# Optimization experiments

Hardware: AMD Instinct MI355X
Metric: run time of the kernel (lower is better)

Reference implementation:

```python
import jax, jax.numpy as jnp
import numpy as np

K = 1024      # num_embeddings
D = 256       # embedding_dim
B, T = 64, 2048
DECAY = 0.99
EPS = 1e-5
COMMIT = 0.25


def setup_inputs() -> dict:
    key = jax.random.key(0)
    k1, k2, k3 = jax.random.split(key, 3)
    inputs = jax.random.normal(k1, (D, B, T), dtype=jnp.float32)
    embedding = jax.random.normal(k2, (K, D), dtype=jnp.float32)        # nn.Embedding weight (normal_())
    ema_w = jax.random.normal(k3, (K, D), dtype=jnp.float32)            # _ema_w (normal_())
    ema_cluster_size = jnp.zeros((K,), dtype=jnp.float32)               # _ema_cluster_size buffer
    return {"inputs": inputs, "embedding": embedding,
            "ema_cluster_size": ema_cluster_size, "ema_w": ema_w}


def reference(inputs, embedding, ema_cluster_size, ema_w):
    # inputs: [D, B, T] -> permute(1,2,0) -> [B, T, D]
    x = jnp.transpose(inputs, (1, 2, 0))
    flat = x.reshape(-1, D)                                  # [N, D], N = B*T

    # squared-euclidean distances to codebook: [N, K]
    distances = (jnp.sum(flat * flat, axis=1, keepdims=True)
                 + jnp.sum(embedding * embedding, axis=1)
                 - 2.0 * (flat @ embedding.T))

    encoding_indices = jnp.argmin(distances, axis=1)         # [N]
    encodings = jax.nn.one_hot(encoding_indices, K, dtype=jnp.float32)  # [N, K]

    # --- EMA codebook update (training path; detached in torch via nn.Parameter rewrap) ---
    counts = jnp.sum(encodings, axis=0)                      # [K]
    new_cs = ema_cluster_size * DECAY + (1.0 - DECAY) * counts
    n = jnp.sum(new_cs)
    new_cs = (new_cs + EPS) / (n + K * EPS) * n              # Laplace smoothing
    dw = encodings.T @ flat                                  # [K, D] scatter-add of assigned vectors
    new_ema_w = ema_w * DECAY + (1.0 - DECAY) * dw
    new_embedding = new_ema_w / new_cs[:, None]              # updated codebook

    # quantize with the UPDATED codebook (as in the torch training path)
    quantized = (encodings @ new_embedding).reshape(x.shape)  # [B, T, D]

    e_latent_loss = jnp.mean((jax.lax.stop_gradient(quantized) - x) ** 2)
    vq_loss = COMMIT * e_latent_loss

    # straight-through estimator
    quantized_st = x + jax.lax.stop_gradient(quantized - x)

    avg_probs = jnp.mean(encodings, axis=0)                  # [K]
    perplexity = jnp.exp(-jnp.sum(avg_probs * jnp.log(avg_probs + 1e-10)))

    quantized_out = jnp.transpose(quantized_st, (2, 0, 1))   # back to [D, B, T]
    return (vq_loss, quantized_out, perplexity, encodings, distances,
            encoding_indices, new_cs, new_ema_w, new_embedding)
```

## Files before the change

kernel.cpp:

```cpp
#include <hip/hip_runtime.h>
#include <hip/hip_bf16.h>
#include <cstdint>
#include <cstddef>

#define N_ROWS 131072
#define K_CB   1024
#define D_DIM  256
#define ND_TOT 33554432ull
#define NK_TOT 134217728ull
#define CHUNK  64

typedef __attribute__((ext_vector_type(8))) short short8;
typedef __attribute__((ext_vector_type(4))) float f32x4;
typedef __attribute__((address_space(3))) uint32_t lds_u32_t;
typedef const __attribute__((address_space(1))) uint32_t glb_u32_t;

static __device__ __forceinline__ float omd() { return (float)(1.0 - 0.99); }

static __device__ __forceinline__ float bf2f(ushort u) {
  union { uint32_t i; float f; } x; x.i = ((uint32_t)u) << 16; return x.f;
}
static __device__ __forceinline__ ushort f2bf(float f) {
  uint32_t x = __builtin_bit_cast(uint32_t, f);
  return (ushort)((x + 0x7fffu + ((x >> 16) & 1u)) >> 16);
}
static __device__ __forceinline__ void split3(float v, ushort& h, ushort& m, ushort& l) {
  h = f2bf(v);
  float r1 = v - bf2f(h);
  m = f2bf(r1);
  l = f2bf(r1 - bf2f(m));
}

__global__ __launch_bounds__(256) void split_a_k(const float* __restrict__ in,
    ushort* __restrict__ aH, ushort* __restrict__ aM, ushort* __restrict__ aL,
    float* __restrict__ xsq) {
  __shared__ float tile[128][65];
  __shared__ float part[4][64];
  int n0 = blockIdx.x * 64, d0 = blockIdx.y * 128;
  int lane = threadIdx.x & 63, grp = threadIdx.x >> 6;
  float ps = 0.f;
#pragma unroll
  for (int r = 0; r < 32; ++r) {
    int d = grp * 32 + r;
    float v = in[(size_t)(d0 + d) * N_ROWS + n0 + lane];
    tile[d][lane] = v;
    ps += v * v;
  }
  part[grp][lane] = ps;
  __syncthreads();
  if (grp == 0) {
    float s = part[0][lane] + part[1][lane] + part[2][lane] + part[3][lane];
    atomicAdd(&xsq[n0 + lane], s);
  }
#pragma unroll
  for (int r = 0; r < 16; ++r) {
    int nr = grp * 16 + r;
    float v0 = tile[lane * 2][nr], v1 = tile[lane * 2 + 1][nr];
    ushort h0, m0, l0, h1, m1, l1;
    split3(v0, h0, m0, l0);
    split3(v1, h1, m1, l1);
    size_t o = (size_t)(n0 + nr) * D_DIM + d0 + lane * 2;
    *(uint32_t*)&aH[o] = (uint32_t)h0 | ((uint32_t)h1 << 16);
    *(uint32_t*)&aM[o] = (uint32_t)m0 | ((uint32_t)m1 << 16);
    *(uint32_t*)&aL[o] = (uint32_t)l0 | ((uint32_t)l1 << 16);
  }
}

__global__ __launch_bounds__(256) void split_b_esq_k(const float* __restrict__ emb,
    ushort* __restrict__ bH, ushort* __restrict__ bM, float* __restrict__ esq) {
  int k = blockIdx.x * 4 + (threadIdx.x >> 6);
  int lane = threadIdx.x & 63;
  const float* er = emb + (size_t)k * D_DIM;
  float s = 0.f;
#pragma unroll
  for (int j = 0; j < 4; ++j) {
    float v = er[j * 64 + lane];
    ushort h, m, l;
    split3(v, h, m, l);
    bH[(size_t)k * D_DIM + j * 64 + lane] = h;
    bM[(size_t)k * D_DIM + j * 64 + lane] = m;
    s += v * v;
  }
  for (int off = 32; off; off >>= 1) s += __shfl_down(s, off);
  if (lane == 0) esq[k] = s;
}

__global__ __launch_bounds__(512, 1) void mfma_dist_k(
    const ushort* __restrict__ aH, const ushort* __restrict__ aM,
    const ushort* __restrict__ bH, const ushort* __restrict__ bM,
    const float* __restrict__ xsq, const float* __restrict__ esq,
    float* __restrict__ dist, float* __restrict__ pminv, int* __restrict__ pmink) {
  extern __shared__ __align__(16) char lds[];
  const int tid = threadIdx.x;
  const int wid = tid >> 6, l = tid & 63;
  const int l15 = l & 15, l4 = l >> 4;
  const int wm = wid >> 2, wn = wid & 3;

  int t0 = ((int)blockIdx.x & 7) * 256 + ((int)blockIdx.x >> 3);
  const int bx = t0 >> 2, by = t0 & 3;
  const int n0 = bx * 256, k0c = by * 256;

  int gOff[4], lOffA[4], lOffB[4];
#pragma unroll
  for (int i = 0; i < 4; ++i) {
    int ch = i * 512 + tid;
    int r = ch >> 3, s = ch & 7;
    gOff[i] = r * 512 + ((s ^ (r & 7)) << 4);
    lOffA[i] = ch << 4;
    lOffB[i] = 32768 + (ch << 4);
  }

  const char* aPl[2] = { (const char*)aH + (size_t)n0 * 512,
                         (const char*)aM + (size_t)n0 * 512 };
  const char* bPl[2] = { (const char*)bH + (size_t)k0c * 512,
                         (const char*)bM + (size_t)k0c * 512 };

  f32x4 acc[8][4];
#pragma unroll
  for (int mi = 0; mi < 8; ++mi)
#pragma unroll
    for (int ni = 0; ni < 4; ++ni)
#pragma unroll
      for (int e = 0; e < 4; ++e) acc[mi][ni][e] = 0.f;

#define STAGE(buf, kt)                                                          \
  {                                                                             \
    const char* pa = aPl[(kt) >> 3] + (((kt) & 3) << 7);                        \
    const char* pb = bPl[((kt) >> 2) & 1] + (((kt) & 3) << 7);                  \
    char* lb = lds + (buf) * 65536;                                             \
    _Pragma("unroll")                                                           \
    for (int i = 0; i < 4; ++i) {                                               \
      __builtin_amdgcn_global_load_lds((glb_u32_t*)(pa + gOff[i]),              \
          (lds_u32_t*)(lb + lOffA[i]), 16, 0, 0);                               \
      __builtin_amdgcn_global_load_lds((glb_u32_t*)(pb + gOff[i]),              \
          (lds_u32_t*)(lb + lOffB[i]), 16, 0, 0);                               \
    }                                                                           \
  }

#define COMPUTE(buf)                                                            \
  {                                                                             \
    const char* LA = lds + (buf) * 65536;                                       \
    const char* LB = LA + 32768;                                                \
    _Pragma("unroll")                                                           \
    for (int ks = 0; ks < 2; ++ks) {                                            \
      const int c = (ks << 2) + l4;                                             \
      short8 bfr[4];                                                            \
      _Pragma("unroll")                                                         \
      for (int ni = 0; ni < 4; ++ni) {                                          \
        int row = wn * 64 + ni * 16 + l15;                                      \
        bfr[ni] = *(const short8*)(LB + row * 128 + ((c ^ (row & 7)) << 4));    \
      }                                                                         \
      _Pragma("unroll")                                                         \
      for (int mi = 0; mi < 8; ++mi) {                                          \
        int row = wm * 128 + mi * 16 + l15;                                     \
        short8 af = *(const short8*)(LA + row * 128 + ((c ^ (row & 7)) << 4));  \
        _Pragma("unroll")                                                       \
        for (int ni = 0; ni < 4; ++ni)                                          \
          acc[mi][ni] = __builtin_amdgcn_mfma_f32_16x16x32_bf16(af, bfr[ni],    \
                                                                acc[mi][ni], 0, 0, 0); \
      }                                                                         \
    }                                                                           \
  }

  STAGE(0, 0);
  __syncthreads();
  for (int kt = 0; kt < 16; ++kt) {
    if (kt < 15) STAGE((kt + 1) & 1, kt + 1);
    COMPUTE(kt & 1);
    __syncthreads();
  }
#undef STAGE
#undef COMPUTE

  float es[4];
#pragma unroll
  for (int ni = 0; ni < 4; ++ni) es[ni] = esq[k0c + wn * 64 + ni * 16 + l15];
  const int slot = by * 4 + wn;

#pragma unroll
  for (int mi = 0; mi < 8; ++mi) {
    float mv[4];
    int mk[4];
#pragma unroll
    for (int reg = 0; reg < 4; ++reg) { mv[reg] = INFINITY; mk[reg] = 0x7fffffff; }
#pragma unroll
    for (int reg = 0; reg < 4; ++reg) {
      int grow = n0 + wm * 128 + mi * 16 + l4 * 4 + reg;
      float xs = xsq[grow];
#pragma unroll
      for (int ni = 0; ni < 4; ++ni) {
        int gcol = k0c + wn * 64 + ni * 16 + l15;
        float dv = xs + es[ni] - 2.f * acc[mi][ni][reg];
        dist[(size_t)grow * K_CB + gcol] = dv;
        if (dv < mv[reg]) { mv[reg] = dv; mk[reg] = gcol; }
      }
    }
#pragma unroll
    for (int off = 1; off < 16; off <<= 1) {
#pragma unroll
      for (int reg = 0; reg < 4; ++reg) {
        float ov = __shfl_xor(mv[reg], off);
        int ok = __shfl_xor(mk[reg], off);
        if (ov < mv[reg] || (ov == mv[reg] && ok < mk[reg])) { mv[reg] = ov; mk[reg] = ok; }
      }
    }
    if (l15 == 0) {
#pragma unroll
      for (int reg = 0; reg < 4; ++reg) {
        int grow = n0 + wm * 128 + mi * 16 + l4 * 4 + reg;
        pminv[(size_t)slot * N_ROWS + grow] = mv[reg];
        pmink[(size_t)slot * N_ROWS + grow] = mk[reg];
      }
    }
  }
}

__global__ __launch_bounds__(256) void argc_k(const float* __restrict__ pminv,
                                              const int* __restrict__ pmink,
                                              int* __restrict__ idx, float* __restrict__ idxf,
                                              unsigned* __restrict__ counts) {
  __shared__ unsigned h[K_CB];
  for (int i = threadIdx.x; i < K_CB; i += 256) h[i] = 0;
  __syncthreads();
  int n = blockIdx.x * 256 + threadIdx.x;
  float mv = INFINITY;
  int mi = 0x7fffffff;
#pragma unroll
  for (int s = 0; s < 16; ++s) {
    float v = pminv[(size_t)s * N_ROWS + n];
    int k = pmink[(size_t)s * N_ROWS + n];
    if (v < mv || (v == mv && k < mi)) { mv = v; mi = k; }
  }
  idx[n] = mi;
  idxf[n] = (float)mi;
  atomicAdd(&h[mi], 1u);
  __syncthreads();
  for (int i = threadIdx.x; i < K_CB; i += 256) {
    unsigned v = h[i];
    if (v) atomicAdd(&counts[i], v);
  }
}

__global__ __launch_bounds__(1024) void prefix_k(const unsigned* __restrict__ counts,
                                                 int* __restrict__ start, int* __restrict__ cursor) {
  __shared__ int s[K_CB];
  int t = threadIdx.x;
  int v = (int)counts[t];
  s[t] = v;
  __syncthreads();
  for (int off = 1; off < K_CB; off <<= 1) {
    int x = (t >= off) ? s[t - off] : 0;
    __syncthreads();
    s[t] += x;
    __syncthreads();
  }
  int excl = s[t] - v;
  start[t] = excl;
  cursor[t] = excl;
  if (t == K_CB - 1) start[K_CB] = s[t];
}

__global__ __launch_bounds__(256) void scatter_k(const int* __restrict__ idx,
                                                 int* __restrict__ cursor, int* __restrict__ sorted) {
  int n = blockIdx.x * 256 + threadIdx.x;
  int pos = atomicAdd(&cursor[idx[n]], 1);
  sorted[pos] = n;
}

__global__ __launch_bounds__(256) void dwc_k(const ushort* __restrict__ aH,
                                             const ushort* __restrict__ aM,
                                             const ushort* __restrict__ aL,
                                             const int* __restrict__ sorted,
                                             const int* __restrict__ idx,
                                             float* __restrict__ dw) {
  __shared__ int s_n[CHUNK];
  __shared__ int s_k[CHUNK];
  int t = threadIdx.x;
  int r0 = blockIdx.x * CHUNK;
  if (t < CHUNK) {
    int n = sorted[r0 + t];
    s_n[t] = n;
    s_k[t] = idx[n];
  }
  __syncthreads();
  float acc = 0.f;
  for (int rb = 0; rb < CHUNK; rb += 8) {
    float v[8];
#pragma unroll
    for (int i = 0; i < 8; ++i) {
      size_t o = (size_t)s_n[rb + i] * D_DIM + t;
      v[i] = bf2f(aH[o]) + bf2f(aM[o]) + bf2f(aL[o]);
    }
#pragma unroll
    for (int i = 0; i < 8; ++i) {
      int r = rb + i;
      acc += v[i];
      if (r == CHUNK - 1 || s_k[r + 1] != s_k[r]) {
        atomicAdd(&dw[(size_t)s_k[r] * D_DIM + t], acc);
        acc = 0.f;
      }
    }
  }
}

__global__ __launch_bounds__(256) void enc_k(const int* __restrict__ idx, float* __restrict__ enc) {
  int n = blockIdx.x * 2 + (threadIdx.x >> 7);
  int c = (threadIdx.x & 127) * 8;
  int k = idx[n];
  float4 a = {0.f, 0.f, 0.f, 0.f}, b = {0.f, 0.f, 0.f, 0.f};
  if (k >= c && k < c + 4) ((float*)&a)[k - c] = 1.0f;
  else if (k >= c + 4 && k < c + 8) ((float*)&b)[k - c - 4] = 1.0f;
  size_t o = (size_t)n * K_CB + c;
  *(float4*)&enc[o] = a;
  *(float4*)&enc[o + 4] = b;
}

__global__ __launch_bounds__(1024) void newcs_k(const float* __restrict__ ema_cs,
                                                const unsigned* __restrict__ counts,
                                                float* __restrict__ out_ncs,
                                                float* __restrict__ out_perp) {
  __shared__ float s[1024];
  int k = threadIdx.x;
  float c = (float)counts[k];
  float raw = 0.99f * ema_cs[k] + omd() * c;
  s[k] = raw;
  __syncthreads();
  for (int off = 512; off; off >>= 1) { if (k < off) s[k] += s[k + off]; __syncthreads(); }
  float nsum = s[0];
  __syncthreads();
  out_ncs[k] = (raw + 1e-5f) / (nsum + (float)(1024 * 1e-5)) * nsum;
  float p = c * (1.0f / 131072.0f);
  float t = p * logf(p + 1e-10f);
  s[k] = t;
  __syncthreads();
  for (int off = 512; off; off >>= 1) { if (k < off) s[k] += s[k + off]; __syncthreads(); }
  if (k == 0) out_perp[0] = expf(-s[0]);
}

__global__ __launch_bounds__(256) void newemb_k(const float* __restrict__ ema_w,
                                                const float* __restrict__ dw,
                                                const float* __restrict__ ncs,
                                                float* __restrict__ out_nw,
                                                float* __restrict__ out_ne) {
  int i = blockIdx.x * 256 + threadIdx.x;
  int k = i >> 8;
  float nw = 0.99f * ema_w[i] + omd() * dw[i];
  out_nw[i] = nw;
  out_ne[i] = nw / ncs[k];
}

__global__ __launch_bounds__(256) void quant_k(const float* __restrict__ in,
                                               const int* __restrict__ idx,
                                               const float* __restrict__ ne,
                                               float* __restrict__ qout,
                                               float* __restrict__ lossacc) {
  float lacc = 0.f;
  size_t stride = (size_t)gridDim.x * 256;
  for (size_t g = (size_t)blockIdx.x * 256 + threadIdx.x; g < (ND_TOT >> 2); g += stride) {
    size_t i = g << 2;
    int d = (int)(i >> 17);
    int n = (int)(i & (N_ROWS - 1));
    float4 x = *(const float4*)&in[i];
    int4 k4 = *(const int4*)&idx[n];
    float4 q;
    q.x = ne[(size_t)k4.x * D_DIM + d];
    q.y = ne[(size_t)k4.y * D_DIM + d];
    q.z = ne[(size_t)k4.z * D_DIM + d];
    q.w = ne[(size_t)k4.w * D_DIM + d];
    float4 o;
    o.x = x.x + (q.x - x.x);
    o.y = x.y + (q.y - x.y);
    o.z = x.z + (q.z - x.z);
    o.w = x.w + (q.w - x.w);
    *(float4*)&qout[i] = o;
    float dx = q.x - x.x, dy = q.y - x.y, dz = q.z - x.z, dwv = q.w - x.w;
    lacc += dx * dx + dy * dy + dz * dz + dwv * dwv;
  }
  for (int off = 32; off; off >>= 1) lacc += __shfl_down(lacc, off);
  __shared__ float w4[4];
  if ((threadIdx.x & 63) == 0) w4[threadIdx.x >> 6] = lacc;
  __syncthreads();
  if (threadIdx.x == 0) atomicAdd(lossacc, w4[0] + w4[1] + w4[2] + w4[3]);
}

__global__ void fin_k(const float* __restrict__ lossacc, float* __restrict__ out_loss) {
  out_loss[0] = 0.25f * lossacc[0] * (1.0f / 33554432.0f);
}

extern "C" void kernel_launch(void* const* d_in, const int* in_sizes, int n_in,
                              void* d_out, int out_size, void* d_ws, size_t ws_size,
                              hipStream_t stream) {
  const float* in     = (const float*)d_in[0];
  const float* emb    = (const float*)d_in[1];
  const float* ema_cs = (const float*)d_in[2];
  const float* ema_w  = (const float*)d_in[3];

  float* out = (float*)d_out;
  float* out_loss = out;
  float* out_q    = out + 1;
  float* out_perp = out + 33554433;
  float* out_enc  = out + 33554434;
  float* out_dist = out + 167772162;
  float* out_idx  = out + 301989890;
  float* out_ncs  = out + 302120962;
  float* out_nw   = out + 302121986;
  float* out_ne   = out + 302384130;

  char* w = (char*)d_ws;
  unsigned* counts  = (unsigned*)(w);
  float*    lossacc = (float*)(w + 4096);
  int*      cursor  = (int*)(w + 8192);
  int*      start   = (int*)(w + 12288);
  float*    xsq     = (float*)(w + 20480);
  float*    esq     = (float*)(w + 544768);
  int*      idx     = (int*)(w + 548864);
  int*      sorted  = (int*)(w + 1073152);
  float*    dw      = (float*)(w + 1597440);

  ushort* aH = (ushort*)((char*)out_enc + 8);
  ushort* aM = aH + ND_TOT;
  ushort* aL = aM + ND_TOT;
  ushort* bH = aL + ND_TOT;
  ushort* bM = bH + (K_CB * D_DIM);
  float*  pminv = (float*)(bM + (K_CB * D_DIM));
  int*    pmink = (int*)(pminv + 16 * (size_t)N_ROWS);

  hipMemsetAsync(d_ws, 0, 544768, stream);
  hipMemsetAsync(dw, 0, K_CB * D_DIM * 4, stream);

  split_a_k<<<dim3(N_ROWS / 64, 2), 256, 0, stream>>>(in, aH, aM, aL, xsq);
  split_b_esq_k<<<K_CB / 4, 256, 0, stream>>>(emb, bH, bM, esq);
  mfma_dist_k<<<(N_ROWS / 256) * (K_CB / 256), 512, 131072, stream>>>(
      aH, aM, bH, bM, xsq, esq, out_dist, pminv, pmink);
  argc_k<<<N_ROWS / 256, 256, 0, stream>>>(pminv, pmink, idx, out_idx, counts);
  prefix_k<<<1, 1024, 0, stream>>>(counts, start, cursor);
  scatter_k<<<N_ROWS / 256, 256, 0, stream>>>(idx, cursor, sorted);
  dwc_k<<<N_ROWS / CHUNK, 256, 0, stream>>>(aH, aM, aL, sorted, idx, dw);
  enc_k<<<N_ROWS / 2, 256, 0, stream>>>(idx, out_enc);
  newcs_k<<<1, 1024, 0, stream>>>(ema_cs, counts, out_ncs, out_perp);
  newemb_k<<<K_CB * D_DIM / 256, 256, 0, stream>>>(ema_w, dw, out_ncs, out_nw, out_ne);
  quant_k<<<2048, 256, 0, stream>>>(in, idx, out_ne, out_q, lossacc);
  fin_k<<<1, 1, 0, stream>>>(lossacc, out_loss);
}
```

Before: 1.008 ms.

## Prefetch two stages ahead with explicit vmcnt waits and MFMA priority

Restructures the distance GEMM main loop so that two K-tiles are staged into LDS up front. Each next stage is issued right after the current buffer is consumed, and waits use explicit s_waitcnt vmcnt counts in place of full __syncthreads. A-fragments are now loaded into registers before the MFMA burst, and s_setprio raises wave priority while the MFMAs issue. The aim is to hide global-to-LDS latency and interleave waves better, at the cost of more registers for the A-fragments and reliance on hand-counted vmcnt values.

```diff
diff --git a/kernel.cpp b/kernel.cpp
--- a/kernel.cpp
+++ b/kernel.cpp
@@ -137,40 +137,55 @@
     }                                                                           \
   }
 
-#define COMPUTE(buf)                                                            \
+#define COMPUTE_KS(buf, ks)                                                     \
   {                                                                             \
     const char* LA = lds + (buf) * 65536;                                       \
     const char* LB = LA + 32768;                                                \
+    const int c = ((ks) << 2) + l4;                                             \
+    short8 bfr[4];                                                              \
     _Pragma("unroll")                                                           \
-    for (int ks = 0; ks < 2; ++ks) {                                            \
-      const int c = (ks << 2) + l4;                                             \
-      short8 bfr[4];                                                            \
+    for (int ni = 0; ni < 4; ++ni) {                                            \
+      int row = wn * 64 + ni * 16 + l15;                                        \
+      bfr[ni] = *(const short8*)(LB + row * 128 + ((c ^ (row & 7)) << 4));      \
+    }                                                                           \
+    short8 afr[8];                                                              \
+    _Pragma("unroll")                                                           \
+    for (int mi = 0; mi < 8; ++mi) {                                            \
+      int row = wm * 128 + mi * 16 + l15;                                       \
+      afr[mi] = *(const short8*)(LA + row * 128 + ((c ^ (row & 7)) << 4));      \
+    }                                                                           \
+    __builtin_amdgcn_s_setprio(1);                                              \
+    _Pragma("unroll")                                                           \
+    for (int mi = 0; mi < 8; ++mi)                                              \
       _Pragma("unroll")                                                         \
-      for (int ni = 0; ni < 4; ++ni) {                                          \
-        int row = wn * 64 + ni * 16 + l15;                                      \
-        bfr[ni] = *(const short8*)(LB + row * 128 + ((c ^ (row & 7)) << 4));    \
-      }                                                                         \
-      _Pragma("unroll")                                                         \
-      for (int mi = 0; mi < 8; ++mi) {                                          \
-        int row = wm * 128 + mi * 16 + l15;                                     \
-        short8 af = *(const short8*)(LA + row * 128 + ((c ^ (row & 7)) << 4));  \
-        _Pragma("unroll")                                                       \
-        for (int ni = 0; ni < 4; ++ni)                                          \
-          acc[mi][ni] = __builtin_amdgcn_mfma_f32_16x16x32_bf16(af, bfr[ni],    \
-                                                                acc[mi][ni], 0, 0, 0); \
-      }                                                                         \
-    }                                                                           \
+      for (int ni = 0; ni < 4; ++ni)                                            \
+        acc[mi][ni] = __builtin_amdgcn_mfma_f32_16x16x32_bf16(afr[mi], bfr[ni], \
+                                                              acc[mi][ni], 0, 0, 0); \
+    __builtin_amdgcn_s_setprio(0);                                              \
   }
 
   STAGE(0, 0);
-  __syncthreads();
+  STAGE(1, 1);
+  asm volatile("s_waitcnt vmcnt(8)" ::: "memory");
+  __builtin_amdgcn_sched_barrier(0);
+  __builtin_amdgcn_s_barrier();
+
   for (int kt = 0; kt < 16; ++kt) {
-    if (kt < 15) STAGE((kt + 1) & 1, kt + 1);
-    COMPUTE(kt & 1);
-    __syncthreads();
+    const int cur = kt & 1;
+    COMPUTE_KS(cur, 0);
+    __builtin_amdgcn_s_barrier();
+    COMPUTE_KS(cur, 1);
+    __builtin_amdgcn_s_barrier();
+    if (kt + 2 < 16) STAGE(cur, kt + 2);
+    if (kt < 15) {
+      if (kt + 2 < 16) { asm volatile("s_waitcnt vmcnt(8)" ::: "memory"); }
+      else             { asm volatile("s_waitcnt vmcnt(0)" ::: "memory"); }
+      __builtin_amdgcn_sched_barrier(0);
+      __builtin_amdgcn_s_barrier();
+    }
   }
 #undef STAGE
-#undef COMPUTE
+#undef COMPUTE_KS
 
   float es[4];
 #pragma unroll
```

Result: slower. 1.043 ms (+3.4%).
